# Performance work log

Measured on AMD Instinct MI355X. Metric: run time of the kernel, lower is better.

The kernel has to match this reference:

```python
import jax, jax.numpy as jnp
import numpy as np

N, E = 100000, 1600000
IN_C, HID, OUT_C = 128, 128, 64
HOPS, L = 2, 3
EPS = 1e-5


def setup_inputs() -> dict:
    key = jax.random.key(0)
    ks = jax.random.split(key, 16)
    x = jax.random.normal(ks[0], (N, IN_C), jnp.float32)
    edge_index = jax.random.randint(ks[1], (2, E), 0, N, dtype=jnp.int32).astype(jnp.int64)
    CAT = HID * (HOPS + 1)  # 384
    def lin(k, fan_in, fan_out, nstack):
        return jax.random.normal(k, (nstack, fan_in, fan_out), jnp.float32) / np.sqrt(fan_in)
    return {
        "x": x,
        "edge_index": edge_index,
        "W0": lin(ks[2], IN_C, HID, HOPS + 1),
        "b0": jnp.zeros((HOPS + 1, HID), jnp.float32),
        "W1": lin(ks[3], CAT, HID, HOPS + 1),
        "b1": jnp.zeros((HOPS + 1, HID), jnp.float32),
        "W2": lin(ks[4], CAT, OUT_C, HOPS + 1),
        "b2": jnp.zeros((HOPS + 1, OUT_C), jnp.float32),
        "bn0_g": jnp.ones((CAT,), jnp.float32),
        "bn0_b": jnp.zeros((CAT,), jnp.float32),
        "bn1_g": jnp.ones((CAT,), jnp.float32),
        "bn1_b": jnp.zeros((CAT,), jnp.float32),
        "fpW": jax.random.normal(ks[5], (OUT_C * (HOPS + 1), OUT_C), jnp.float32) / np.sqrt(OUT_C * (HOPS + 1)),
        "fpb": jnp.zeros((OUT_C,), jnp.float32),
    }


def reference(x, edge_index, W0, b0, W1, b1, W2, b2,
              bn0_g, bn0_b, bn1_g, bn1_b, fpW, fpb):
    row, col = edge_index[0], edge_index[1]
    # gcn_norm with add_self_loops=False, unit edge weights:
    # deg = scatter_add(1, col); w_e = deg^-1/2[row] * deg^-1/2[col]
    deg = jnp.zeros((N,), x.dtype).at[col].add(1.0)
    dinv = jnp.where(deg > 0, jax.lax.rsqrt(jnp.maximum(deg, 1.0)), 0.0)
    ew = dinv[row] * dinv[col]

    def spmm(h):
        # adj_t = SparseTensor(row=col, col=row, value=ew): out[col] += ew * h[row]
        return jax.ops.segment_sum(ew[:, None] * h[row], col, num_segments=N)

    def mixhop(h, W, b):
        outs = []
        for j in range(HOPS + 1):
            hj = h @ W[j] + b[j]          # lins[j](h)
            for _ in range(j):
                hj = spmm(hj)             # A^j applied j times
            outs.append(hj)
        return jnp.concatenate(outs, axis=1)

    def bn(h, g, bb):
        # BatchNorm1d in training mode: batch stats, biased variance
        mu = h.mean(axis=0)
        var = h.var(axis=0)
        return g * (h - mu) * jax.lax.rsqrt(var + EPS) + bb

    h = jax.nn.relu(bn(mixhop(x, W0, b0), bn0_g, bn0_b))   # dropout: identity (eval)
    h = jax.nn.relu(bn(mixhop(h, W1, b1), bn1_g, bn1_b))
    h = mixhop(h, W2, b2)
    return h @ fpW + fpb
```

## Files before the change

### kernel.cpp

```cpp
#include <hip/hip_runtime.h>
#include <cstdint>
#include <cstddef>

#define IN_C 128
#define HIDc 128
#define OUTc 64

using bf8 = __attribute__((ext_vector_type(8))) __bf16;
using f4  = __attribute__((ext_vector_type(4))) float;

__device__ __forceinline__ unsigned short f2bf(float f) {
    unsigned int u = __float_as_uint(f);
    unsigned int r = (u + 0x7FFFu + ((u >> 16) & 1u)) >> 16;
    return (unsigned short)r;
}
__device__ __forceinline__ float bf2f(unsigned short h) {
    return __uint_as_float(((unsigned int)h) << 16);
}

__device__ __forceinline__ void gload16(const unsigned short* g, unsigned short* l) {
    __builtin_amdgcn_global_load_lds(
        (const __attribute__((address_space(1))) unsigned int*)g,
        (__attribute__((address_space(3))) unsigned int*)l, 16, 0, 0);
}

__global__ void k_detect(const long long* ei, int n_nodes, int* flag) {
    int t = threadIdx.x;
    long long v = ei[t];
    int ok = (v >= 0 && v < (long long)n_nodes) ? 1 : 0;
    unsigned long long m = __ballot(ok);
    if (t == 0) *flag = (m == ~0ull) ? 1 : 0;
}

__global__ void k_cvt_hist(const void* ei, int twoE, int E, const int* flag,
                           int* __restrict__ out, int* __restrict__ deg, int n) {
    int i = blockIdx.x * blockDim.x + threadIdx.x;
    if (i >= twoE) return;
    int v = (*flag) ? (int)((const long long*)ei)[i] : ((const int*)ei)[i];
    out[i] = v;
    if (i >= E && (unsigned)v < (unsigned)n) atomicAdd(&deg[v], 1);
}

__global__ void k_dinv(const int* __restrict__ deg, float* __restrict__ dinv, int n) {
    int i = blockIdx.x * blockDim.x + threadIdx.x;
    if (i < n) dinv[i] = (deg[i] > 0) ? rsqrtf((float)deg[i]) : 0.0f;
}

__global__ void k_alloc(const int* __restrict__ deg, int* __restrict__ base,
                        int* __restrict__ cursor, int* __restrict__ counter, int n) {
    int i = blockIdx.x * blockDim.x + threadIdx.x;
    int lane = threadIdx.x & 63;
    int val = (i < n) ? deg[i] : 0;
    int scan = val;
    #pragma unroll
    for (int off = 1; off < 64; off <<= 1) {
        int t = __shfl_up(scan, off);
        if (lane >= off) scan += t;
    }
    int excl = scan - val;
    int total = __shfl(scan, 63);
    int wb = 0;
    if (lane == 0) wb = atomicAdd(counter, total);
    wb = __shfl(wb, 0);
    if (i < n) { base[i] = wb + excl; cursor[i] = wb + excl; }
}

__global__ void k_scatter(const int* __restrict__ eint, int E,
                          const float* __restrict__ dinv, int n,
                          int* __restrict__ cursor, int2* __restrict__ ew) {
    int e = blockIdx.x * blockDim.x + threadIdx.x;
    if (e >= E) return;
    int r = eint[e];
    int c = eint[E + e];
    if ((unsigned)r >= (unsigned)n || (unsigned)c >= (unsigned)n) return;
    int p = atomicAdd(&cursor[c], 1);
    int2 v; v.x = r; v.y = __float_as_int(dinv[r] * dinv[c]);
    ew[p] = v;
}

__global__ void k_wprep(const float* __restrict__ W, unsigned short* __restrict__ Wt,
                        int K, int N) {
    int j = blockIdx.y;
    int idx = blockIdx.x * 256 + threadIdx.x;
    if (idx >= K * N) return;
    int k = idx / N, nn = idx - k * N;
    Wt[(size_t)j * N * K + (size_t)nn * K + k] = f2bf(W[(size_t)j * K * N + idx]);
}

__global__ void k_cast4(const float* __restrict__ x, unsigned short* __restrict__ y, int n4) {
    int i = blockIdx.x * 256 + threadIdx.x;
    if (i >= n4) return;
    float4 v = ((const float4*)x)[i];
    ushort4 o;
    o.x = f2bf(v.x); o.y = f2bf(v.y); o.z = f2bf(v.z); o.w = f2bf(v.w);
    ((ushort4*)y)[i] = o;
}

template<int TILEN, bool BFOUT>
__global__ __launch_bounds__(256) void k_gemm(
    const unsigned short* __restrict__ A0, const unsigned short* __restrict__ A1,
    const unsigned short* __restrict__ A2, int W, int M, int K,
    const unsigned short* __restrict__ Bt,
    const float* __restrict__ bias,
    unsigned short* __restrict__ C0, int ldc0,
    unsigned short* __restrict__ C1, int ldc1,
    unsigned short* __restrict__ C2, int ldc2,
    float* __restrict__ Cf, int ldcf)
{
    constexpr int TM = 4;
    constexpr int TN = TILEN / 32;
    __shared__ __align__(16) unsigned short As[128 * 32];
    __shared__ __align__(16) unsigned short Bs[TILEN * 32];
    __shared__ __align__(16) unsigned char  Cs[16384];

    int t = threadIdx.x;
    int wave = t >> 6, lane = t & 63;
    int m16 = lane & 15, q = lane >> 4;
    int j = blockIdx.y;
    int row0 = blockIdx.x * 128;
    int wr = (wave & 1) * 64;
    int wc = (wave >> 1) * (TILEN / 2);

    int lr = lane >> 2, lch = lane & 3;
    int ra0 = (wave * 2 + 0) * 16 + lr;
    int ra1 = (wave * 2 + 1) * 16 + lr;
    int ga0 = row0 + ra0; if (ga0 >= M) ga0 = M - 1;
    int ga1 = row0 + ra1; if (ga1 >= M) ga1 = M - 1;
    size_t boff0 = (size_t)(j * TILEN + ra0) * K;
    size_t boff1 = (size_t)(j * TILEN + ra1) * K;
    size_t boffS = (size_t)(j * TILEN + wave * 16 + lr) * K;

    f4 acc[TM][TN];
    #pragma unroll
    for (int i = 0; i < TM; i++)
        #pragma unroll
        for (int jj = 0; jj < TN; jj++) acc[i][jj] = (f4){0.f, 0.f, 0.f, 0.f};

    for (int kk = 0; kk < K; kk += 32) {
        int pi = kk / W;
        const unsigned short* Ap = (pi == 0) ? A0 : ((pi == 1) ? A1 : A2);
        int kl = kk - pi * W;

        __syncthreads();
        gload16(&Ap[(size_t)ga0 * W + kl + lch * 8], &As[(wave * 2 + 0) * 512]);
        gload16(&Ap[(size_t)ga1 * W + kl + lch * 8], &As[(wave * 2 + 1) * 512]);
        if (TILEN == 128) {
            gload16(&Bt[boff0 + kk + lch * 8], &Bs[(wave * 2 + 0) * 512]);
            gload16(&Bt[boff1 + kk + lch * 8], &Bs[(wave * 2 + 1) * 512]);
        } else {
            gload16(&Bt[boffS + kk + lch * 8], &Bs[wave * 512]);
        }
        __syncthreads();

        bf8 af[TM], bfr[TN];
        #pragma unroll
        for (int tm = 0; tm < TM; tm++)
            af[tm] = *(const bf8*)&As[(wr + tm * 16 + m16) * 32 + q * 8];
        #pragma unroll
        for (int tn = 0; tn < TN; tn++)
            bfr[tn] = *(const bf8*)&Bs[(wc + tn * 16 + m16) * 32 + q * 8];
        #pragma unroll
        for (int tm = 0; tm < TM; tm++)
            #pragma unroll
            for (int tn = 0; tn < TN; tn++)
                acc[tm][tn] = __builtin_amdgcn_mfma_f32_16x16x32_bf16(
                    af[tm], bfr[tn], acc[tm][tn], 0, 0, 0);
    }

    constexpr int EB  = BFOUT ? 2 : 4;
    constexpr int RB  = TILEN * EB;
    constexpr int CPR = RB / 16;
    constexpr int PT  = 64 * CPR / 256;
    char* Cb;
    long  ldb;
    if (BFOUT) {
        unsigned short* Cj = (j == 0) ? C0 : ((j == 1) ? C1 : C2);
        int lj = (j == 0) ? ldc0 : ((j == 1) ? ldc1 : ldc2);
        Cb = (char*)Cj; ldb = (long)lj * 2;
    } else {
        Cb = (char*)Cf; ldb = (long)ldcf * 4;
    }
    #pragma unroll
    for (int half = 0; half < 2; half++) {
        __syncthreads();
        if ((wave & 1) == half) {
            #pragma unroll
            for (int tn = 0; tn < TN; tn++) {
                int col = wc + tn * 16 + m16;
                float bi = bias[j * TILEN + col];
                #pragma unroll
                for (int tm = 0; tm < TM; tm++) {
                    #pragma unroll
                    for (int r = 0; r < 4; r++) {
                        int lrow = tm * 16 + q * 4 + r;
                        float v = acc[tm][tn][r] + bi;
                        if (BFOUT) ((unsigned short*)Cs)[lrow * TILEN + col] = f2bf(v);
                        else       ((float*)Cs)[lrow * TILEN + col] = v;
                    }
                }
            }
        }
        __syncthreads();
        #pragma unroll
        for (int i = 0; i < PT; i++) {
            int idx  = i * 256 + t;
            int lrow = idx / CPR;
            int c16  = idx - lrow * CPR;
            int grow = row0 + half * 64 + lrow;
            if (grow < M)
                *(uint4*)(Cb + (size_t)grow * ldb + c16 * 16) = ((const uint4*)Cs)[idx];
        }
    }
}

template<int PW>
__global__ __launch_bounds__(256) void k_spmm2i(
    const unsigned short* __restrict__ S,
    unsigned short* __restrict__ D1, unsigned short* __restrict__ D2,
    const int* __restrict__ base, const int* __restrict__ deg,
    const int2* __restrict__ ew, int n)
{
    int node = blockIdx.x * 4 + threadIdx.y;
    if (node >= n) return;
    int lane = threadIdx.x;
    constexpr int CV = PW / 32;
    int half = lane >> 5, lx = lane & 31;
    const unsigned short* Sp = S + half * PW + lx * CV;
    float acc[CV];
    #pragma unroll
    for (int v = 0; v < CV; v++) acc[v] = 0.f;
    int b = base[node], end = b + deg[node];
    constexpr int UN = 8;
    int e = b;
    for (; e + UN <= end; e += UN) {
        int2 ev[UN];
        #pragma unroll
        for (int u = 0; u < UN; u++) ev[u] = ew[e + u];
        ushort4 g4[UN]; ushort2 g2[UN];
        #pragma unroll
        for (int u = 0; u < UN; u++) {
            if (CV == 4) g4[u] = *(const ushort4*)(Sp + (size_t)ev[u].x * (2 * PW));
            else         g2[u] = *(const ushort2*)(Sp + (size_t)ev[u].x * (2 * PW));
        }
        #pragma unroll
        for (int u = 0; u < UN; u++) {
            float we = __int_as_float(ev[u].y);
            if (CV == 4) {
                acc[0] += we * bf2f(g4[u].x); acc[1] += we * bf2f(g4[u].y);
                acc[2] += we * bf2f(g4[u].z); acc[3] += we * bf2f(g4[u].w);
            } else {
                acc[0] += we * bf2f(g2[u].x); acc[1] += we * bf2f(g2[u].y);
            }
        }
    }
    for (; e < end; ++e) {
        int2 ev = ew[e];
        float we = __int_as_float(ev.y);
        if (CV == 4) {
            ushort4 g = *(const ushort4*)(Sp + (size_t)ev.x * (2 * PW));
            acc[0] += we * bf2f(g.x); acc[1] += we * bf2f(g.y);
            acc[2] += we * bf2f(g.z); acc[3] += we * bf2f(g.w);
        } else {
            ushort2 g = *(const ushort2*)(Sp + (size_t)ev.x * (2 * PW));
            acc[0] += we * bf2f(g.x); acc[1] += we * bf2f(g.y);
        }
    }
    unsigned short* D = half ? D2 : D1;
    size_t o = (size_t)node * PW + lx * CV;
    if (CV == 4) {
        ushort4 ov;
        ov.x = f2bf(acc[0]); ov.y = f2bf(acc[1]);
        ov.z = f2bf(acc[2]); ov.w = f2bf(acc[3]);
        *(ushort4*)&D[o] = ov;
    } else {
        ushort2 ov; ov.x = f2bf(acc[0]); ov.y = f2bf(acc[1]);
        *(ushort2*)&D[o] = ov;
    }
}

template<int V>
__global__ __launch_bounds__(256) void k_spmm(
    const unsigned short* __restrict__ S1, unsigned short* __restrict__ D1, int width,
    const int* __restrict__ base, const int* __restrict__ deg,
    const int2* __restrict__ ew, int n)
{
    int node = blockIdx.x * 4 + threadIdx.y;
    if (node >= n) return;
    int tx = threadIdx.x;
    float a1[V];
    #pragma unroll
    for (int v = 0; v < V; v++) a1[v] = 0.f;
    int b = base[node], end = b + deg[node];
    const unsigned short* P1 = S1 + tx * V;
    constexpr int UN = 8;
    int e = b;
    for (; e + UN <= end; e += UN) {
        int2 ev[UN];
        #pragma unroll
        for (int u = 0; u < UN; u++) ev[u] = ew[e + u];
        unsigned int g1[UN];
        #pragma unroll
        for (int u = 0; u < UN; u++) {
            if (V == 2) g1[u] = *(const unsigned int*)(P1 + (size_t)ev[u].x * width);
            else        g1[u] = P1[(size_t)ev[u].x * width];
        }
        #pragma unroll
        for (int u = 0; u < UN; u++) {
            float we = __int_as_float(ev[u].y);
            if (V == 2) {
                a1[0] += we * bf2f((unsigned short)(g1[u] & 0xffff));
                a1[1] += we * bf2f((unsigned short)(g1[u] >> 16));
            } else {
                a1[0] += we * bf2f((unsigned short)g1[u]);
            }
        }
    }
    for (; e < end; ++e) {
        int2 ev = ew[e];
        float we = __int_as_float(ev.y);
        if (V == 2) {
            unsigned int u1 = *(const unsigned int*)(P1 + (size_t)ev.x * width);
            a1[0] += we * bf2f((unsigned short)(u1 & 0xffff));
            a1[1] += we * bf2f((unsigned short)(u1 >> 16));
        } else {
            a1[0] += we * bf2f(P1[(size_t)ev.x * width]);
        }
    }
    size_t o = (size_t)node * width + tx * V;
    if (V == 2) {
        ushort2 o1; o1.x = f2bf(a1[0]); o1.y = f2bf(a1[1]);
        *(ushort2*)&D1[o] = o1;
    } else {
        D1[o] = f2bf(a1[0]);
    }
}

__global__ void k_bnstats(const unsigned short* __restrict__ p0,
                          const unsigned short* __restrict__ p1,
                          const unsigned short* __restrict__ p2,
                          float* __restrict__ sums, float* __restrict__ sumsq, int n)
{
    int c = threadIdx.x;
    int cc = c & 127;
    int pi = c >> 7;
    const unsigned short* src = (pi == 0) ? p0 : ((pi == 1) ? p1 : p2);
    float s = 0.f, s2 = 0.f;
    for (int r = blockIdx.x; r < n; r += gridDim.x) {
        float v = bf2f(src[(size_t)r * 128 + cc]);
        s += v; s2 += v * v;
    }
    atomicAdd(&sums[c], s);
    atomicAdd(&sumsq[c], s2);
}

__global__ void k_bnfin(const float* __restrict__ sums, const float* __restrict__ sumsq,
                        const float* __restrict__ g, const float* __restrict__ bb,
                        float* __restrict__ scale, float* __restrict__ shift,
                        int cat, float invn)
{
    int c = threadIdx.x;
    if (c >= cat) return;
    float mu  = sums[c] * invn;
    float var = sumsq[c] * invn - mu * mu;
    float sc  = g[c] * rsqrtf(var + 1e-5f);
    scale[c] = sc;
    shift[c] = bb[c] - mu * sc;
}

__global__ void k_bnapply(unsigned short* __restrict__ p0, unsigned short* __restrict__ p1,
                          unsigned short* __restrict__ p2,
                          const float* __restrict__ scale, const float* __restrict__ shift,
                          int n)
{
    int c = threadIdx.x;
    int cc = c & 127;
    int pi = c >> 7;
    unsigned short* src = (pi == 0) ? p0 : ((pi == 1) ? p1 : p2);
    float sc = scale[c], sh = shift[c];
    for (int r = blockIdx.x; r < n; r += gridDim.x) {
        size_t idx = (size_t)r * 128 + cc;
        float v = bf2f(src[idx]) * sc + sh;
        src[idx] = f2bf(fmaxf(v, 0.0f));
    }
}

__global__ void k_diag(float* out, float val, int n) {
    int i = blockIdx.x * blockDim.x + threadIdx.x;
    if (i < n) out[i] = val;
}

extern "C" void kernel_launch(void* const* d_in, const int* in_sizes, int n_in,
                              void* d_out, int out_size, void* d_ws, size_t ws_size,
                              hipStream_t stream)
{
    const float* x    = (const float*)d_in[0];
    const void*  ei   = d_in[1];
    const float* W0   = (const float*)d_in[2];
    const float* b0   = (const float*)d_in[3];
    const float* W1   = (const float*)d_in[4];
    const float* b1   = (const float*)d_in[5];
    const float* W2   = (const float*)d_in[6];
    const float* b2   = (const float*)d_in[7];
    const float* bn0g = (const float*)d_in[8];
    const float* bn0b = (const float*)d_in[9];
    const float* bn1g = (const float*)d_in[10];
    const float* bn1b = (const float*)d_in[11];
    const float* fpW  = (const float*)d_in[12];
    const float* fpb  = (const float*)d_in[13];
    float* out = (float*)d_out;

    const int N    = in_sizes[0] / IN_C;
    const int twoE = in_sizes[1];
    const int E    = twoE / 2;

    char* p = (char*)d_ws;
    auto alloc = [&](size_t bytes) -> char* {
        char* r = p; p += (bytes + 255) & ~(size_t)255; return r;
    };
    unsigned short* u0 = (unsigned short*)alloc((size_t)6 * N * 128 * 2);
    unsigned short* u1 = u0 + (size_t)1 * N * 128;
    unsigned short* u2 = u0 + (size_t)2 * N * 128;
    unsigned short* u3 = u0 + (size_t)3 * N * 128;
    unsigned short* u4 = u0 + (size_t)4 * N * 128;
    unsigned short* u5 = u0 + (size_t)5 * N * 128;
    unsigned short* Wt0 = (unsigned short*)alloc((size_t)3 * 128 * 128 * 2);
    unsigned short* Wt1 = (unsigned short*)alloc((size_t)3 * 384 * 128 * 2);
    unsigned short* Wt2 = (unsigned short*)alloc((size_t)3 * 384 * 64 * 2);
    unsigned short* WtF = (unsigned short*)alloc((size_t)192 * 64 * 2);
    float* dinv  = (float*)alloc((size_t)N * 4);
    int2*  ew    = (int2*)alloc((size_t)E * 8);
    float* sums  = (float*)alloc(2 * 384 * 4);
    float* sumsq = sums + 384;
    float* scale = (float*)alloc(384 * 4);
    float* shift = (float*)alloc(384 * 4);
    int* deg     = (int*)alloc((size_t)N * 4);
    int* base    = (int*)alloc((size_t)N * 4);
    int* cursor  = (int*)alloc((size_t)N * 4);
    int* eint    = (int*)alloc((size_t)twoE * 4);
    int* counter = (int*)alloc(4);
    int* flag    = (int*)alloc(4);

    size_t required = (size_t)(p - (char*)d_ws);
    if (required > ws_size) {
        k_diag<<<(out_size + 255) / 256, 256, 0, stream>>>(
            out, (float)(ws_size >> 20), out_size);
        return;
    }

    const int T = 256;
    dim3 spmm_blk(64, 4);
    int  spmm_grid = (N + 3) / 4;
    int  gx = (N + 127) / 128;

    k_wprep<<<dim3((128 * 128 + 255) / 256, 3), T, 0, stream>>>(W0, Wt0, 128, 128);
    k_wprep<<<dim3((384 * 128 + 255) / 256, 3), T, 0, stream>>>(W1, Wt1, 384, 128);
    k_wprep<<<dim3((384 * 64  + 255) / 256, 3), T, 0, stream>>>(W2, Wt2, 384, 64);
    k_wprep<<<dim3((192 * 64  + 255) / 256, 1), T, 0, stream>>>(fpW, WtF, 192, 64);
    unsigned short* Xb = u3;
    k_cast4<<<((N * 128 / 4) + 255) / 256, T, 0, stream>>>(x, Xb, N * 128 / 4);

    hipMemsetAsync(deg, 0, (size_t)N * 4, stream);
    hipMemsetAsync(counter, 0, 4, stream);
    k_detect<<<1, 64, 0, stream>>>((const long long*)ei, N, flag);
    k_cvt_hist<<<(twoE + T - 1) / T, T, 0, stream>>>(ei, twoE, E, flag, eint, deg, N);
    k_dinv<<<(N + T - 1) / T, T, 0, stream>>>(deg, dinv, N);
    k_alloc<<<(N + T - 1) / T, T, 0, stream>>>(deg, base, cursor, counter, N);
    k_scatter<<<(E + T - 1) / T, T, 0, stream>>>(eint, E, dinv, N, cursor, ew);

    k_gemm<128, true><<<dim3(gx, 3), T, 0, stream>>>(Xb, Xb, Xb, 128, N, 128,
        Wt0, b0, u0, 128, u1, 256, u1 + 128, 256, nullptr, 0);
    k_spmm2i<128><<<spmm_grid, spmm_blk, 0, stream>>>(u1, u4, u5, base, deg, ew, N);
    k_spmm<2><<<spmm_grid, spmm_blk, 0, stream>>>(u5, u3, 128, base, deg, ew, N);
    hipMemsetAsync(sums, 0, 2 * 384 * 4, stream);
    k_bnstats<<<2048, 384, 0, stream>>>(u0, u4, u3, sums, sumsq, N);
    k_bnfin<<<1, 384, 0, stream>>>(sums, sumsq, bn0g, bn0b, scale, shift, 384, 1.0f / N);
    k_bnapply<<<2048, 384, 0, stream>>>(u0, u4, u3, scale, shift, N);

    k_gemm<128, true><<<dim3(gx, 3), T, 0, stream>>>(u0, u4, u3, 128, N, 384,
        Wt1, b1, u5, 128, u1, 256, u1 + 128, 256, nullptr, 0);
    k_spmm2i<128><<<spmm_grid, spmm_blk, 0, stream>>>(u1, u0, u4, base, deg, ew, N);
    k_spmm<2><<<spmm_grid, spmm_blk, 0, stream>>>(u4, u3, 128, base, deg, ew, N);
    hipMemsetAsync(sums, 0, 2 * 384 * 4, stream);
    k_bnstats<<<2048, 384, 0, stream>>>(u5, u0, u3, sums, sumsq, N);
    k_bnfin<<<1, 384, 0, stream>>>(sums, sumsq, bn1g, bn1b, scale, shift, 384, 1.0f / N);
    k_bnapply<<<2048, 384, 0, stream>>>(u5, u0, u3, scale, shift, N);

    k_gemm<64, true><<<dim3(gx, 3), T, 0, stream>>>(u5, u0, u3, 128, N, 384,
        Wt2, b2, u1, 64, u2, 128, u2 + 64, 128, nullptr, 0);
    k_spmm2i<64><<<spmm_grid, spmm_blk, 0, stream>>>(u2, u4, u4 + (size_t)N * 64,
                                                     base, deg, ew, N);
    k_spmm<1><<<spmm_grid, spmm_blk, 0, stream>>>(u4 + (size_t)N * 64, u5, 64,
                                                  base, deg, ew, N);

    k_gemm<64, false><<<dim3(gx, 1), T, 0, stream>>>(u1, u4, u5, 64, N, 192,
        WtF, fpb, nullptr, 0, nullptr, 0, nullptr, 0, out, 64);
}
```

Before: 1.237 ms.

## Split SpMM edges across lane groups with 16-byte gathers and shuffle reduction

Both SpMM kernels are rewritten so that each wavefront splits a node's edges across several lane subgroups. Each lane gathers 16 bytes (8 bf16 values) per edge row, and the partial sums are combined with xor shuffles before one group writes the result. Previously each lane loaded only 4-8 bytes per edge and walked all edges serially. The aim is fewer, wider memory transactions and more gathers in flight per node. In exchange it adds shuffle-reduction overhead, clamped loads that waste work on padded tail slots, and more registers per lane.

```diff
diff --git a/kernel.cpp b/kernel.cpp
--- a/kernel.cpp
+++ b/kernel.cpp
@@ -214,124 +214,137 @@
 }
 
 template<int PW>
-__global__ __launch_bounds__(256) void k_spmm2i(
+__global__ __launch_bounds__(256) void k_spmm2v(
     const unsigned short* __restrict__ S,
     unsigned short* __restrict__ D1, unsigned short* __restrict__ D2,
     const int* __restrict__ base, const int* __restrict__ deg,
     const int2* __restrict__ ew, int n)
 {
+    constexpr int ROWB = 2 * PW;
+    constexpr int GS   = ROWB / 8;
+    constexpr int EP   = 64 / GS;
+    constexpr int UN   = 16 / EP;
+
     int node = blockIdx.x * 4 + threadIdx.y;
     if (node >= n) return;
     int lane = threadIdx.x;
-    constexpr int CV = PW / 32;
-    int half = lane >> 5, lx = lane & 31;
-    const unsigned short* Sp = S + half * PW + lx * CV;
-    float acc[CV];
-    #pragma unroll
-    for (int v = 0; v < CV; v++) acc[v] = 0.f;
-    int b = base[node], end = b + deg[node];
-    constexpr int UN = 8;
-    int e = b;
-    for (; e + UN <= end; e += UN) {
-        int2 ev[UN];
-        #pragma unroll
-        for (int u = 0; u < UN; u++) ev[u] = ew[e + u];
-        ushort4 g4[UN]; ushort2 g2[UN];
-        #pragma unroll
-        for (int u = 0; u < UN; u++) {
-            if (CV == 4) g4[u] = *(const ushort4*)(Sp + (size_t)ev[u].x * (2 * PW));
-            else         g2[u] = *(const ushort2*)(Sp + (size_t)ev[u].x * (2 * PW));
-        }
-        #pragma unroll
-        for (int u = 0; u < UN; u++) {
-            float we = __int_as_float(ev[u].y);
-            if (CV == 4) {
-                acc[0] += we * bf2f(g4[u].x); acc[1] += we * bf2f(g4[u].y);
-                acc[2] += we * bf2f(g4[u].z); acc[3] += we * bf2f(g4[u].w);
-            } else {
-                acc[0] += we * bf2f(g2[u].x); acc[1] += we * bf2f(g2[u].y);
+    int sub  = lane / GS;
+    int li   = lane % GS;
+    const unsigned short* Sp = S + li * 8;
+
+    float acc[8];
+    #pragma unroll
+    for (int v = 0; v < 8; v++) acc[v] = 0.f;
+
+    int b = base[node], d = deg[node];
+    if (d > 0) {
+        int end = b + d;
+        for (int e = b; e < end; e += UN * EP) {
+            int row[UN]; float wt[UN];
+            #pragma unroll
+            for (int u = 0; u < UN; u++) {
+                int myE = e + u * EP + sub;
+                int cl  = myE < end ? myE : end - 1;
+                int2 ev = ew[cl];
+                row[u] = ev.x;
+                wt[u]  = (myE < end) ? __int_as_float(ev.y) : 0.f;
+            }
+            uint4 g[UN];
+            #pragma unroll
+            for (int u = 0; u < UN; u++)
+                g[u] = *(const uint4*)(Sp + (size_t)row[u] * ROWB);
+            #pragma unroll
+            for (int u = 0; u < UN; u++) {
+                float we = wt[u];
+                const unsigned int* gw = (const unsigned int*)&g[u];
+                #pragma unroll
+                for (int p = 0; p < 4; p++) {
+                    acc[2 * p]     += we * bf2f((unsigned short)(gw[p] & 0xffff));
+                    acc[2 * p + 1] += we * bf2f((unsigned short)(gw[p] >> 16));
+                }
             }
         }
     }
-    for (; e < end; ++e) {
-        int2 ev = ew[e];
-        float we = __int_as_float(ev.y);
-        if (CV == 4) {
-            ushort4 g = *(const ushort4*)(Sp + (size_t)ev.x * (2 * PW));
-            acc[0] += we * bf2f(g.x); acc[1] += we * bf2f(g.y);
-            acc[2] += we * bf2f(g.z); acc[3] += we * bf2f(g.w);
-        } else {
-            ushort2 g = *(const ushort2*)(Sp + (size_t)ev.x * (2 * PW));
-            acc[0] += we * bf2f(g.x); acc[1] += we * bf2f(g.y);
-        }
-    }
-    unsigned short* D = half ? D2 : D1;
-    size_t o = (size_t)node * PW + lx * CV;
-    if (CV == 4) {
-        ushort4 ov;
-        ov.x = f2bf(acc[0]); ov.y = f2bf(acc[1]);
-        ov.z = f2bf(acc[2]); ov.w = f2bf(acc[3]);
-        *(ushort4*)&D[o] = ov;
-    } else {
-        ushort2 ov; ov.x = f2bf(acc[0]); ov.y = f2bf(acc[1]);
-        *(ushort2*)&D[o] = ov;
-    }
-}
-
-template<int V>
-__global__ __launch_bounds__(256) void k_spmm(
-    const unsigned short* __restrict__ S1, unsigned short* __restrict__ D1, int width,
+    #pragma unroll
+    for (int m = GS; m < 64; m <<= 1)
+        #pragma unroll
+        for (int v = 0; v < 8; v++) acc[v] += __shfl_xor(acc[v], m);
+
+    if (lane < GS) {
+        int cu = li * 8;
+        unsigned short* D = (cu < PW) ? (D1 + (size_t)node * PW + cu)
+                                      : (D2 + (size_t)node * PW + (cu - PW));
+        uint4 o;
+        o.x = (unsigned)f2bf(acc[0]) | ((unsigned)f2bf(acc[1]) << 16);
+        o.y = (unsigned)f2bf(acc[2]) | ((unsigned)f2bf(acc[3]) << 16);
+        o.z = (unsigned)f2bf(acc[4]) | ((unsigned)f2bf(acc[5]) << 16);
+        o.w = (unsigned)f2bf(acc[6]) | ((unsigned)f2bf(acc[7]) << 16);
+        *(uint4*)D = o;
+    }
+}
+
+template<int W>
+__global__ __launch_bounds__(256) void k_spmmv(
+    const unsigned short* __restrict__ S, unsigned short* __restrict__ D,
     const int* __restrict__ base, const int* __restrict__ deg,
     const int2* __restrict__ ew, int n)
 {
+    constexpr int GS = W / 8;
+    constexpr int EP = 64 / GS;
+    constexpr int UN = (EP == 4) ? 4 : 2;
+
     int node = blockIdx.x * 4 + threadIdx.y;
     if (node >= n) return;
-    int tx = threadIdx.x;
-    float a1[V];
-    #pragma unroll
-    for (int v = 0; v < V; v++) a1[v] = 0.f;
-    int b = base[node], end = b + deg[node];
-    const unsigned short* P1 = S1 + tx * V;
-    constexpr int UN = 8;
-    int e = b;
-    for (; e + UN <= end; e += UN) {
-        int2 ev[UN];
-        #pragma unroll
-        for (int u = 0; u < UN; u++) ev[u] = ew[e + u];
-        unsigned int g1[UN];
-        #pragma unroll
-        for (int u = 0; u < UN; u++) {
-            if (V == 2) g1[u] = *(const unsigned int*)(P1 + (size_t)ev[u].x * width);
-            else        g1[u] = P1[(size_t)ev[u].x * width];
-        }
-        #pragma unroll
-        for (int u = 0; u < UN; u++) {
-            float we = __int_as_float(ev[u].y);
-            if (V == 2) {
-                a1[0] += we * bf2f((unsigned short)(g1[u] & 0xffff));
-                a1[1] += we * bf2f((unsigned short)(g1[u] >> 16));
-            } else {
-                a1[0] += we * bf2f((unsigned short)g1[u]);
+    int lane = threadIdx.x;
+    int sub  = lane / GS;
+    int li   = lane % GS;
+    const unsigned short* Sp = S + li * 8;
+
+    float acc[8];
+    #pragma unroll
+    for (int v = 0; v < 8; v++) acc[v] = 0.f;
+
+    int b = base[node], d = deg[node];
+    if (d > 0) {
+        int end = b + d;
+        for (int e = b; e < end; e += UN * EP) {
+            int row[UN]; float wt[UN];
+            #pragma unroll
+            for (int u = 0; u < UN; u++) {
+                int myE = e + u * EP + sub;
+                int cl  = myE < end ? myE : end - 1;
+                int2 ev = ew[cl];
+                row[u] = ev.x;
+                wt[u]  = (myE < end) ? __int_as_float(ev.y) : 0.f;
+            }
+            uint4 g[UN];
+            #pragma unroll
+            for (int u = 0; u < UN; u++)
+                g[u] = *(const uint4*)(Sp + (size_t)row[u] * W);
+            #pragma unroll
+            for (int u = 0; u < UN; u++) {
+                float we = wt[u];
+                const unsigned int* gw = (const unsigned int*)&g[u];
+                #pragma unroll
+                for (int p = 0; p < 4; p++) {
+                    acc[2 * p]     += we * bf2f((unsigned short)(gw[p] & 0xffff));
+                    acc[2 * p + 1] += we * bf2f((unsigned short)(gw[p] >> 16));
+                }
             }
         }
     }
-    for (; e < end; ++e) {
-        int2 ev = ew[e];
-        float we = __int_as_float(ev.y);
-        if (V == 2) {
-            unsigned int u1 = *(const unsigned int*)(P1 + (size_t)ev.x * width);
-            a1[0] += we * bf2f((unsigned short)(u1 & 0xffff));
-            a1[1] += we * bf2f((unsigned short)(u1 >> 16));
-        } else {
-            a1[0] += we * bf2f(P1[(size_t)ev.x * width]);
-        }
-    }
-    size_t o = (size_t)node * width + tx * V;
-    if (V == 2) {
-        ushort2 o1; o1.x = f2bf(a1[0]); o1.y = f2bf(a1[1]);
-        *(ushort2*)&D1[o] = o1;
-    } else {
-        D1[o] = f2bf(a1[0]);
+    #pragma unroll
+    for (int m = GS; m < 64; m <<= 1)
+        #pragma unroll
+        for (int v = 0; v < 8; v++) acc[v] += __shfl_xor(acc[v], m);
+
+    if (lane < GS) {
+        uint4 o;
+        o.x = (unsigned)f2bf(acc[0]) | ((unsigned)f2bf(acc[1]) << 16);
+        o.y = (unsigned)f2bf(acc[2]) | ((unsigned)f2bf(acc[3]) << 16);
+        o.z = (unsigned)f2bf(acc[4]) | ((unsigned)f2bf(acc[5]) << 16);
+        o.w = (unsigned)f2bf(acc[6]) | ((unsigned)f2bf(acc[7]) << 16);
+        *(uint4*)(D + (size_t)node * W + li * 8) = o;
     }
 }
 
@@ -469,8 +482,8 @@
 
     k_gemm<128, true><<<dim3(gx, 3), T, 0, stream>>>(Xb, Xb, Xb, 128, N, 128,
         Wt0, b0, u0, 128, u1, 256, u1 + 128, 256, nullptr, 0);
-    k_spmm2i<128><<<spmm_grid, spmm_blk, 0, stream>>>(u1, u4, u5, base, deg, ew, N);
-    k_spmm<2><<<spmm_grid, spmm_blk, 0, stream>>>(u5, u3, 128, base, deg, ew, N);
+    k_spmm2v<128><<<spmm_grid, spmm_blk, 0, stream>>>(u1, u4, u5, base, deg, ew, N);
+    k_spmmv<128><<<spmm_grid, spmm_blk, 0, stream>>>(u5, u3, base, deg, ew, N);
     hipMemsetAsync(sums, 0, 2 * 384 * 4, stream);
     k_bnstats<<<2048, 384, 0, stream>>>(u0, u4, u3, sums, sumsq, N);
     k_bnfin<<<1, 384, 0, stream>>>(sums, sumsq, bn0g, bn0b, scale, shift, 384, 1.0f / N);
@@ -478,8 +491,8 @@
 
     k_gemm<128, true><<<dim3(gx, 3), T, 0, stream>>>(u0, u4, u3, 128, N, 384,
         Wt1, b1, u5, 128, u1, 256, u1 + 128, 256, nullptr, 0);
-    k_spmm2i<128><<<spmm_grid, spmm_blk, 0, stream>>>(u1, u0, u4, base, deg, ew, N);
-    k_spmm<2><<<spmm_grid, spmm_blk, 0, stream>>>(u4, u3, 128, base, deg, ew, N);
+    k_spmm2v<128><<<spmm_grid, spmm_blk, 0, stream>>>(u1, u0, u4, base, deg, ew, N);
+    k_spmmv<128><<<spmm_grid, spmm_blk, 0, stream>>>(u4, u3, base, deg, ew, N);
     hipMemsetAsync(sums, 0, 2 * 384 * 4, stream);
     k_bnstats<<<2048, 384, 0, stream>>>(u5, u0, u3, sums, sumsq, N);
     k_bnfin<<<1, 384, 0, stream>>>(sums, sumsq, bn1g, bn1b, scale, shift, 384, 1.0f / N);
@@ -487,10 +500,10 @@
 
     k_gemm<64, true><<<dim3(gx, 3), T, 0, stream>>>(u5, u0, u3, 128, N, 384,
         Wt2, b2, u1, 64, u2, 128, u2 + 64, 128, nullptr, 0);
-    k_spmm2i<64><<<spmm_grid, spmm_blk, 0, stream>>>(u2, u4, u4 + (size_t)N * 64,
+    k_spmm2v<64><<<spmm_grid, spmm_blk, 0, stream>>>(u2, u4, u4 + (size_t)N * 64,
                                                      base, deg, ew, N);
-    k_spmm<1><<<spmm_grid, spmm_blk, 0, stream>>>(u4 + (size_t)N * 64, u5, 64,
-                                                  base, deg, ew, N);
+    k_spmmv<64><<<spmm_grid, spmm_blk, 0, stream>>>(u4 + (size_t)N * 64, u5,
+                                                    base, deg, ew, N);
 
     k_gemm<64, false><<<dim3(gx, 1), T, 0, stream>>>(u1, u4, u5, 64, N, 192,
         WtF, fpb, nullptr, 0, nullptr, 0, nullptr, 0, out, 64);
```

New measurement: 1.139 ms. -7.9%, faster.
